# Optimization experiments

Measured on AMD Instinct MI355X. Metric: run time of the kernel, lower is better.

## Reference

```python
import jax, jax.numpy as jnp
import numpy as np

MAX_ITER = 3  # matches init max_iter
# structures exercised: sib_be, sib_bb, cop, grd, split (all distinct branches)


def _mfvi(s_const, s_arg_begin, s_arg_end,
          s_sib_be, s_sib_eb, s_sib_bb, s_sib_ee,
          s_cop_b, s_cop_e, s_grd_b, s_grd_e, s_split,
          edge_mask, chart_mask):
    B, S, _ = edge_mask.shape
    idx = jnp.arange(S)
    hs = jnp.broadcast_to(idx[:, None], (S, S))   # hs[i,j] = i (head index)
    ms = jnp.broadcast_to(idx[None, :], (S, S))   # ms[i,j] = j (modifier index)
    ls, rs = jnp.minimum(hs, ms), jnp.maximum(hs, ms)

    c0 = chart_mask[:, 0]
    pad_mask = c0[:, :, None] & c0[:, None, :]           # [B,j,k]
    chart = jnp.roll(chart_mask, 1, axis=1)              # cat((chart[:,-1:], chart[:,:-1]), 1)

    # [B,i,j,k] = edge[b,i,j] & edge[b,i,k]
    mask2o_base = edge_mask[:, :, :, None] & edge_mask[:, :, None, :]
    ne_hk = (hs[:, :, None] != idx)                      # i != k
    mask2o_wm = mask2o_base & ne_hk[None]
    mask2o = mask2o_wm & (ms[:, :, None] != idx)[None]   # additionally j != k

    lhs = ls[None, :, :] >= hs[:, :, None]               # min(j,k) >= i
    rhs = rs[None, :, :] <= hs[:, :, None]               # max(j,k) <= i
    triu_jk = idx[:, None] <= idx[None, :]               # keep k >= j (torch .triu())
    noncross = mask2o_wm & (triu_jk[None, None] & (lhs | rhs)[None])

    span_m2o = (chart[:, :, :, None]
                & (rs[:, :, None] != idx)[None]          # max(i,j) != k
                & pad_mask[:, None, :, :])
    inside = (hs[:, :, None] <= idx) & (ms[:, :, None] >= idx)  # i<=k<=... & j>=k
    outside = (~inside)[None] & span_m2o

    mzero = lambda s, m: jnp.where(m, s, 0.0)
    s_sib_be_m = mzero(s_sib_be, mask2o_wm)
    s_sib_eb_m = mzero(s_sib_eb, jnp.swapaxes(mask2o_wm, -2, -1))
    s_sib_bb_m = mzero(s_sib_bb, mask2o)
    s_sib_ee_m = mzero(s_sib_ee, mask2o)
    s_cop_b_m = mzero(s_cop_b, mask2o)
    s_cop_e_m = mzero(s_cop_e, mask2o)
    s_edge_grd_b = mzero(s_grd_b, noncross)
    s_edge_grd_e = mzero(s_grd_e, jnp.swapaxes(noncross, -2, -1))
    s_span_grd_b = mzero(jnp.transpose(s_grd_b, (0, 2, 3, 1)), outside)
    s_span_grd_e = mzero(jnp.transpose(s_grd_e, (0, 3, 2, 1)), outside)
    s_split_m = mzero(s_split, span_m2o)

    # NOTE: the torch code does `tmp_q_b = s_arg_begin; tmp_q_b += ...`, which
    # mutates the base score tensors in place, so messages ACCUMULATE into the
    # bases across iterations. We reproduce that semantics here.
    base_b, base_e, base_s = s_arg_begin, s_arg_end, s_const
    q_b, q_e, q_s = base_b, base_e, base_s
    for _ in range(MAX_ITER):
        qb = jax.nn.sigmoid(q_b)
        qe = jax.nn.sigmoid(q_e)
        qs = jax.nn.sigmoid(q_s)
        base_b = (base_b
                  + jnp.einsum('bik,bijk->bij', qe, s_sib_be_m)
                  + jnp.einsum('bik,bijk->bij', qb, s_sib_bb_m)
                  + jnp.einsum('bkj,bijk->bij', qb, s_cop_b_m)
                  + jnp.einsum('bjk,bijk->bij', qs, s_edge_grd_b))
        base_e = (base_e
                  + jnp.einsum('bik,bijk->bij', qb, s_sib_eb_m)
                  + jnp.einsum('bik,bijk->bij', qe, s_sib_ee_m)
                  + jnp.einsum('bkj,bijk->bij', qe, s_cop_e_m)
                  + jnp.einsum('bkj,bijk->bij', qs, s_edge_grd_e))
        base_s = (base_s
                  + jnp.einsum('bki,bijk->bij', qb, s_span_grd_b)
                  + jnp.einsum('bkj,bijk->bij', qe, s_span_grd_e)
                  + jnp.einsum('bik,bijk->bij', qs, s_split_m))
        q_b, q_e, q_s = base_b, base_e, base_s
    return q_b, q_e, q_s


def setup_inputs() -> dict:
    key = jax.random.key(0)
    B, S = 4, 128
    ks = jax.random.split(key, 16)
    f3 = lambda k: jax.random.normal(k, (B, S, S), jnp.float32)
    # scale 4D scores down so sums over S stay in a sane sigmoid range
    f4 = lambda k: jax.random.normal(k, (B, S, S, S), jnp.float32) * 0.05
    return {
        's_const': f3(ks[0]),
        's_arg_begin': f3(ks[1]),
        's_arg_end': f3(ks[2]),
        's_sib_be': f4(ks[3]),
        's_sib_eb': f4(ks[4]),
        's_sib_bb': f4(ks[5]),
        's_sib_ee': f4(ks[6]),
        's_cop_b': f4(ks[7]),
        's_cop_e': f4(ks[8]),
        's_grd_b': f4(ks[9]),
        's_grd_e': f4(ks[10]),
        's_split': f4(ks[11]),
        'arg_begin_mask': jax.random.bernoulli(ks[12], 0.5, (B, S, S)),
        'chart_mask': jax.random.bernoulli(ks[13], 0.5, (B, S, S)),
    }


def reference(s_const, s_arg_begin, s_arg_end,
              s_sib_be, s_sib_eb, s_sib_bb, s_sib_ee,
              s_cop_b, s_cop_e, s_grd_b, s_grd_e, s_split,
              arg_begin_mask, chart_mask):
    return _mfvi(s_const, s_arg_begin, s_arg_end,
                 s_sib_be, s_sib_eb, s_sib_bb, s_sib_ee,
                 s_cop_b, s_cop_e, s_grd_b, s_grd_e, s_split,
                 arg_begin_mask, chart_mask)
```

## Files before the change

### kernel.cpp

```cpp
#include <hip/hip_runtime.h>

#define BB 4
#define S 128
#define SS (S*S)
#define BSS (BB*SS)

__device__ __forceinline__ int off3(int b, int i, int j) { return (b * S + i) * S + j; }
__device__ __forceinline__ int off4(int b, int i, int j, int k) { return ((b * S + i) * S + j) * S + k; }

__global__ __launch_bounds__(256) void k_sigmoid(const float* __restrict__ sb,
                                                 const float* __restrict__ se,
                                                 const float* __restrict__ ss,
                                                 float* base,
                                                 float* __restrict__ ws, int init) {
    const int b = blockIdx.z, p = blockIdx.y;
    const int ti = blockIdx.x >> 2, tj = blockIdx.x & 3;
    const int col = threadIdx.x & 31, r0 = threadIdx.x >> 5;
    const float* src = (p == 0) ? sb : (p == 1) ? se : ss;

    __shared__ float tile[32][33];
#pragma unroll
    for (int rr = 0; rr < 4; ++rr) {
        const int row = r0 + 8 * rr;
        const int gi = 32 * ti + row, gj = 32 * tj + col;
        const float x = src[off3(b, gi, gj)];
        const float q = 1.0f / (1.0f + __expf(-x));
        ws[p * BSS + off3(b, gi, gj)] = q;
        if (init) base[p * BSS + off3(b, gi, gj)] = x;
        tile[row][col] = q;
    }
    __syncthreads();
#pragma unroll
    for (int rr = 0; rr < 4; ++rr) {
        const int rowo = r0 + 8 * rr;
        ws[(3 + p) * BSS + off3(b, 32 * tj + rowo, 32 * ti + col)] = tile[col][rowo];
    }
}

__global__ __launch_bounds__(256, 4) void k_terms(
    const float* __restrict__ be, const float* __restrict__ bb,
    const float* __restrict__ cb, const float* __restrict__ eb,
    const float* __restrict__ ee, const float* __restrict__ ce,
    const float* __restrict__ sp, const float* __restrict__ gb,
    const float* __restrict__ ge, const int* __restrict__ edge,
    const int* __restrict__ chart, const float* __restrict__ ws,
    float* __restrict__ base) {
    const int b = blockIdx.z, y = blockIdx.y, x = blockIdx.x;
    const int t = threadIdx.x, hw = t >> 5, lh = t & 31, l = t & 63;
    const int K = 4 * lh;

    const float* qb = ws;
    const float* qe = ws + BSS;
    const float* qs = ws + 2 * BSS;
    const float* qbT = ws + 3 * BSS;
    const float* qeT = ws + 4 * BSS;
    const float* qsT = ws + 5 * BSS;

    if (y < 7) {
        const int I = x;
        const float* A;
        int plane;
        switch (y) {
            case 0: A = be; plane = 0; break;
            case 1: A = bb; plane = 0; break;
            case 2: A = cb; plane = 0; break;
            case 3: A = eb; plane = 1; break;
            case 4: A = ee; plane = 1; break;
            case 5: A = ce; plane = 1; break;
            default: A = sp; plane = 2; break;
        }
        const int Iprev = (I + S - 1) & (S - 1);

        const bool pe0 = edge[off3(b, I, l)] != 0;
        const bool pe1 = edge[off3(b, I, 64 + l)] != 0;
        unsigned long long Mlo = __ballot(pe0), Mhi = __ballot(pe1);
        if (y == 6) {
            const bool pc0 = chart[off3(b, 0, l)] != 0;
            const bool pc1 = chart[off3(b, 0, 64 + l)] != 0;
            const bool ph0 = chart[off3(b, Iprev, l)] != 0;
            const bool ph1 = chart[off3(b, Iprev, 64 + l)] != 0;
            Mlo = __ballot(pc0) & __ballot(ph0);
            Mhi = __ballot(pc1) & __ballot(ph1);
        } else if (y == 3) {
            if (I < 64) Mlo &= ~(1ull << I);
            else Mhi &= ~(1ull << (I - 64));
        }

        const float* qrow = (y == 0 || y == 4) ? qe : (y == 1 || y == 3) ? qb : qs;
        const float4 qv = *(const float4*)&qrow[off3(b, I, K)];
        const int4 ekv = *(const int4*)&edge[off3(b, I, K)];
        const int4 c0kv = *(const int4*)&chart[off3(b, 0, K)];
        float pm[4];
        bool pmask[4];
#pragma unroll
        for (int c = 0; c < 4; ++c) {
            const bool ek = (&ekv.x)[c] != 0;
            const bool c0k = (&c0kv.x)[c] != 0;
            const bool nI = (I != K + c);
            if (y == 0 || y == 1 || y == 4) pm[c] = (ek && nI) ? (&qv.x)[c] : 0.f;
            else if (y == 3) pm[c] = ek ? (&qv.x)[c] : 0.f;
            else if (y == 6) pm[c] = c0k ? (&qv.x)[c] : 0.f;
            pmask[c] = ek && nI;
        }
        const int corrSel = (y == 1 || y == 4) ? 1 : (y == 6) ? 2 : 0;
        const float* qT3 = (y == 2) ? qbT : qeT;

        float acc[16];
        if (y == 2 || y == 5) {
#pragma unroll
            for (int jj = 0; jj < 16; ++jj) {
                const int j = 8 * jj + hw;
                const float4 v = *(const float4*)&A[off4(b, I, j, K)];
                const float4 cf = *(const float4*)&qT3[off3(b, j, K)];
                float dot = 0.f;
                float s[4];
#pragma unroll
                for (int c = 0; c < 4; ++c) {
                    s[c] = pmask[c] ? (&cf.x)[c] : 0.f;
                    dot += s[c] * (&v.x)[c];
                }
#pragma unroll
                for (int c = 0; c < 4; ++c)
                    dot -= (K + c == j) ? s[c] * (&v.x)[c] : 0.f;
                const unsigned long long M = (jj < 8) ? Mlo : Mhi;
                const bool bit = (M >> (((jj & 7) << 3) + hw)) & 1;
                acc[jj] = bit ? dot : 0.f;
            }
        } else {
#pragma unroll
            for (int jj = 0; jj < 16; ++jj) {
                const int j = 8 * jj + hw;
                const float4 v = *(const float4*)&A[off4(b, I, j, K)];
                float dot = pm[0] * v.x + pm[1] * v.y + pm[2] * v.z + pm[3] * v.w;
                const int ci = (corrSel == 0) ? 256 : (corrSel == 1) ? j : (I > j ? I : j);
#pragma unroll
                for (int c = 0; c < 4; ++c)
                    dot -= (K + c == ci) ? pm[c] * (&v.x)[c] : 0.f;
                const unsigned long long M = (jj < 8) ? Mlo : Mhi;
                const bool bit = (M >> (((jj & 7) << 3) + hw)) & 1;
                acc[jj] = bit ? dot : 0.f;
            }
        }

#pragma unroll
        for (int o = 16; o > 0; o >>= 1) {
#pragma unroll
            for (int jj = 0; jj < 16; ++jj) acc[jj] += __shfl_xor(acc[jj], o);
        }
        if (lh == 0) {
#pragma unroll
            for (int jj = 0; jj < 16; ++jj)
                atomicAdd(&base[plane * BSS + off3(b, I, 8 * jj + hw)], acc[jj]);
        }
    } else {
        const float* A = (y == 7) ? gb : ge;
        const float* qT = (y == 7) ? qbT : qeT;
        const int Jt = x & 15, Is = x >> 4;
        const int J = 8 * Jt + hw, I0 = 16 * Is;

        const float4 q_J = (y == 7) ? *(const float4*)&qs[off3(b, J, K)]
                                    : *(const float4*)&qsT[off3(b, J, K)];
        const int4 c0Kv = *(const int4*)&chart[off3(b, 0, K)];
        const bool c0J = chart[off3(b, 0, J)] != 0;
        const int Jprev = (J + S - 1) & (S - 1);
        const int4 chJKv = *(const int4*)&chart[off3(b, Jprev, K)];
        bool c0K[4], chJK[4], chKJ[4];
        int mxJ[4];
#pragma unroll
        for (int c = 0; c < 4; ++c) {
            c0K[c] = (&c0Kv.x)[c] != 0;
            chJK[c] = (&chJKv.x)[c] != 0;
            chKJ[c] = (y == 8) ? (chart[off3(b, (K + c + S - 1) & (S - 1), J)] != 0) : false;
            mxJ[c] = J > (K + c) ? J : (K + c);
        }

        const unsigned long long MeIJ = __ballot(edge[off3(b, I0 + (l & 15), J)] != 0);
        const unsigned long long Mc0I = __ballot(chart[off3(b, 0, I0 + (l & 15))] != 0);
        const int hsh = l & 32;

        float accE[16];
        float rs[4] = {0.f, 0.f, 0.f, 0.f};

#pragma unroll
        for (int s = 0; s < 16; ++s) {
            const int I = I0 + s;
            const float4 v = *(const float4*)&A[off4(b, I, J, K)];
            const int4 eIKv = *(const int4*)&edge[off3(b, I, K)];
            const bool eIJ = (MeIJ >> (hsh + s)) & 1;
            const bool c0I = (Mc0I >> (hsh + s)) & 1;
            const float qT_JI = qT[off3(b, J, I)];

            float p = 0.f;
#pragma unroll
            for (int c = 0; c < 4; ++c) {
                const int Kc = K + c;
                const bool eIK = (&eIKv.x)[c] != 0;
                const float vv = (&v.x)[c];
                bool nc, o;
                if (y == 7) {
                    nc = eIJ && eIK && (I != Kc) && (J <= Kc) && (J >= I || Kc <= I);
                    o = !((J <= I) && (Kc >= I)) && chJK[c] && (mxJ[c] != I) && c0K[c] && c0I;
                } else {
                    nc = eIK && eIJ && (I != J) && (Kc <= J) && (Kc >= I || J <= I);
                    o = !((Kc <= I) && (J >= I)) && chKJ[c] && (mxJ[c] != I) && c0J && c0I;
                }
                p += (nc ? (&q_J.x)[c] : 0.f) * vv;
                rs[c] += (o ? qT_JI : 0.f) * vv;
            }
            accE[s] = p;
        }

#pragma unroll
        for (int o = 16; o > 0; o >>= 1) {
#pragma unroll
            for (int s = 0; s < 16; ++s) accE[s] += __shfl_xor(accE[s], o);
        }
        if (lh == 0) {
#pragma unroll
            for (int s = 0; s < 16; ++s)
                atomicAdd(&base[(y == 7 ? 0 : 1) * BSS + off3(b, I0 + s, J)], accE[s]);
        }

#pragma unroll
        for (int c = 0; c < 4; ++c) {
            if (y == 7)
                atomicAdd(&base[2 * BSS + off3(b, J, K + c)], rs[c]);
            else
                atomicAdd(&base[2 * BSS + off3(b, K + c, J)], rs[c]);
        }
    }
}

extern "C" void kernel_launch(void* const* d_in, const int* in_sizes, int n_in,
                              void* d_out, int out_size, void* d_ws, size_t ws_size,
                              hipStream_t stream) {
    (void)in_sizes; (void)n_in; (void)out_size; (void)ws_size;
    const float* s_const = (const float*)d_in[0];
    const float* s_arg_begin = (const float*)d_in[1];
    const float* s_arg_end = (const float*)d_in[2];
    const float* be = (const float*)d_in[3];
    const float* eb = (const float*)d_in[4];
    const float* bb = (const float*)d_in[5];
    const float* ee = (const float*)d_in[6];
    const float* cb = (const float*)d_in[7];
    const float* ce = (const float*)d_in[8];
    const float* gb = (const float*)d_in[9];
    const float* ge = (const float*)d_in[10];
    const float* sp = (const float*)d_in[11];
    const int* edge = (const int*)d_in[12];
    const int* chart = (const int*)d_in[13];
    float* base = (float*)d_out;
    float* ws = (float*)d_ws;

    for (int it = 0; it < 3; ++it) {
        if (it == 0)
            k_sigmoid<<<dim3(16, 3, BB), dim3(256), 0, stream>>>(s_arg_begin, s_arg_end,
                                                                 s_const, base, ws, 1);
        else
            k_sigmoid<<<dim3(16, 3, BB), dim3(256), 0, stream>>>(base, base + BSS,
                                                                 base + 2 * BSS, base, ws, 0);
        k_terms<<<dim3(S, 9, BB), dim3(256), 0, stream>>>(be, bb, cb, eb, ee, ce, sp, gb, ge,
                                                          edge, chart, ws, base);
    }
}
```

Measured before the change: 500.5 us.

## Replace atomic accumulation with per-block partial planes and merge terms per row

Fuses the three per-plane score contractions sharing the same row into one block, cutting the terms grid from 9 to 5 rows of blocks and sharing the q loads. All atomicAdds into the output are replaced by plain stores into separate workspace partial planes: row sums via a shared-memory buffer, span sums as 16 slices. The sigmoid kernel then reduces those partials into the base scores. A final extra launch folds in the last iteration's partials. This removes atomic contention and makes the result deterministic, at the cost of more workspace traffic and one more launch.

```diff
diff --git a/kernel.cpp b/kernel.cpp
--- a/kernel.cpp
+++ b/kernel.cpp
@@ -5,30 +5,63 @@
 #define SS (S*S)
 #define BSS (BB*SS)
 
+#define WQ_B  0
+#define WQ_E  1
+#define WQ_S  2
+#define WQ_BT 3
+#define WQ_ET 4
+#define WQ_ST 5
+#define WP0   6
+#define WP1   7
+#define WP2   8
+#define WAE0  9
+#define WAE1  10
+#define WRS7  11
+#define WRS8  19
+
 __device__ __forceinline__ int off3(int b, int i, int j) { return (b * S + i) * S + j; }
 __device__ __forceinline__ int off4(int b, int i, int j, int k) { return ((b * S + i) * S + j) * S + k; }
 
 __global__ __launch_bounds__(256) void k_sigmoid(const float* __restrict__ sb,
                                                  const float* __restrict__ se,
                                                  const float* __restrict__ ss,
-                                                 float* base,
-                                                 float* __restrict__ ws, int init) {
+                                                 float* __restrict__ base,
+                                                 float* __restrict__ ws, int mode) {
     const int b = blockIdx.z, p = blockIdx.y;
     const int ti = blockIdx.x >> 2, tj = blockIdx.x & 3;
     const int col = threadIdx.x & 31, r0 = threadIdx.x >> 5;
-    const float* src = (p == 0) ? sb : (p == 1) ? se : ss;
-
     __shared__ float tile[32][33];
+    float* bp = base + p * BSS;
+
 #pragma unroll
     for (int rr = 0; rr < 4; ++rr) {
         const int row = r0 + 8 * rr;
         const int gi = 32 * ti + row, gj = 32 * tj + col;
-        const float x = src[off3(b, gi, gj)];
-        const float q = 1.0f / (1.0f + __expf(-x));
-        ws[p * BSS + off3(b, gi, gj)] = q;
-        if (init) base[p * BSS + off3(b, gi, gj)] = x;
-        tile[row][col] = q;
-    }
+        const int idx = off3(b, gi, gj);
+        float v;
+        if (mode == 0) {
+            const float* src = (p == 0) ? sb : (p == 1) ? se : ss;
+            v = src[idx];
+        } else {
+            v = bp[idx];
+            if (p == 0) {
+                v += ws[WP0 * BSS + idx] + ws[WAE0 * BSS + idx];
+            } else if (p == 1) {
+                v += ws[WP1 * BSS + idx] + ws[WAE1 * BSS + idx];
+            } else {
+                v += ws[WP2 * BSS + idx];
+#pragma unroll
+                for (int n = 0; n < 16; ++n) v += ws[(WRS7 + n) * BSS + idx];
+            }
+        }
+        bp[idx] = v;
+        if (mode < 2) {
+            const float q = 1.0f / (1.0f + __expf(-v));
+            ws[p * BSS + idx] = q;
+            tile[row][col] = q;
+        }
+    }
+    if (mode == 2) return;
     __syncthreads();
 #pragma unroll
     for (int rr = 0; rr < 4; ++rr) {
@@ -37,17 +70,17 @@
     }
 }
 
-__global__ __launch_bounds__(256, 4) void k_terms(
+__global__ __launch_bounds__(256) void k_terms(
     const float* __restrict__ be, const float* __restrict__ bb,
     const float* __restrict__ cb, const float* __restrict__ eb,
     const float* __restrict__ ee, const float* __restrict__ ce,
     const float* __restrict__ sp, const float* __restrict__ gb,
     const float* __restrict__ ge, const int* __restrict__ edge,
-    const int* __restrict__ chart, const float* __restrict__ ws,
-    float* __restrict__ base) {
-    const int b = blockIdx.z, y = blockIdx.y, x = blockIdx.x;
+    const int* __restrict__ chart, float* __restrict__ ws) {
+    const int b = blockIdx.z, yy = blockIdx.y, x = blockIdx.x;
     const int t = threadIdx.x, hw = t >> 5, lh = t & 31, l = t & 63;
     const int K = 4 * lh;
+    __shared__ float rowbuf[128];
 
     const float* qb = ws;
     const float* qe = ws + BSS;
@@ -56,110 +89,107 @@
     const float* qeT = ws + 4 * BSS;
     const float* qsT = ws + 5 * BSS;
 
-    if (y < 7) {
+    if (yy < 3) {
         const int I = x;
-        const float* A;
-        int plane;
-        switch (y) {
-            case 0: A = be; plane = 0; break;
-            case 1: A = bb; plane = 0; break;
-            case 2: A = cb; plane = 0; break;
-            case 3: A = eb; plane = 1; break;
-            case 4: A = ee; plane = 1; break;
-            case 5: A = ce; plane = 1; break;
-            default: A = sp; plane = 2; break;
-        }
-        const int Iprev = (I + S - 1) & (S - 1);
-
-        const bool pe0 = edge[off3(b, I, l)] != 0;
-        const bool pe1 = edge[off3(b, I, 64 + l)] != 0;
-        unsigned long long Mlo = __ballot(pe0), Mhi = __ballot(pe1);
-        if (y == 6) {
-            const bool pc0 = chart[off3(b, 0, l)] != 0;
-            const bool pc1 = chart[off3(b, 0, 64 + l)] != 0;
-            const bool ph0 = chart[off3(b, Iprev, l)] != 0;
-            const bool ph1 = chart[off3(b, Iprev, 64 + l)] != 0;
-            Mlo = __ballot(pc0) & __ballot(ph0);
-            Mhi = __ballot(pc1) & __ballot(ph1);
-        } else if (y == 3) {
-            if (I < 64) Mlo &= ~(1ull << I);
-            else Mhi &= ~(1ull << (I - 64));
-        }
-
-        const float* qrow = (y == 0 || y == 4) ? qe : (y == 1 || y == 3) ? qb : qs;
-        const float4 qv = *(const float4*)&qrow[off3(b, I, K)];
+        unsigned long long Mlo, Mhi;
+        if (yy == 2) {
+            const int Iprev = (I + S - 1) & (S - 1);
+            Mlo = __ballot(chart[off3(b, 0, l)] != 0) & __ballot(chart[off3(b, Iprev, l)] != 0);
+            Mhi = __ballot(chart[off3(b, 0, 64 + l)] != 0) & __ballot(chart[off3(b, Iprev, 64 + l)] != 0);
+        } else {
+            Mlo = __ballot(edge[off3(b, I, l)] != 0);
+            Mhi = __ballot(edge[off3(b, I, 64 + l)] != 0);
+        }
         const int4 ekv = *(const int4*)&edge[off3(b, I, K)];
-        const int4 c0kv = *(const int4*)&chart[off3(b, 0, K)];
-        float pm[4];
-        bool pmask[4];
-#pragma unroll
-        for (int c = 0; c < 4; ++c) {
-            const bool ek = (&ekv.x)[c] != 0;
-            const bool c0k = (&c0kv.x)[c] != 0;
-            const bool nI = (I != K + c);
-            if (y == 0 || y == 1 || y == 4) pm[c] = (ek && nI) ? (&qv.x)[c] : 0.f;
-            else if (y == 3) pm[c] = ek ? (&qv.x)[c] : 0.f;
-            else if (y == 6) pm[c] = c0k ? (&qv.x)[c] : 0.f;
-            pmask[c] = ek && nI;
-        }
-        const int corrSel = (y == 1 || y == 4) ? 1 : (y == 6) ? 2 : 0;
-        const float* qT3 = (y == 2) ? qbT : qeT;
-
         float acc[16];
-        if (y == 2 || y == 5) {
-#pragma unroll
-            for (int jj = 0; jj < 16; ++jj) {
-                const int j = 8 * jj + hw;
-                const float4 v = *(const float4*)&A[off4(b, I, j, K)];
+
+        if (yy == 2) {
+            const int4 c0kv = *(const int4*)&chart[off3(b, 0, K)];
+            const float4 qv = *(const float4*)&qs[off3(b, I, K)];
+            float pm[4];
+#pragma unroll
+            for (int c = 0; c < 4; ++c) pm[c] = ((&c0kv.x)[c] != 0) ? (&qv.x)[c] : 0.f;
+#pragma unroll
+            for (int jj = 0; jj < 16; ++jj) {
+                const int j = 8 * jj + hw;
+                const float4 v = *(const float4*)&sp[off4(b, I, j, K)];
+                float d = pm[0] * v.x + pm[1] * v.y + pm[2] * v.z + pm[3] * v.w;
+                const int ci = I > j ? I : j;
+#pragma unroll
+                for (int c = 0; c < 4; ++c) d -= (K + c == ci) ? pm[c] * (&v.x)[c] : 0.f;
+                acc[jj] = d;
+            }
+        } else {
+            const float4 qbv = *(const float4*)&qb[off3(b, I, K)];
+            const float4 qev = *(const float4*)&qe[off3(b, I, K)];
+            float pmA[4], pmB[4];
+            bool pmk[4];
+#pragma unroll
+            for (int c = 0; c < 4; ++c) {
+                const bool ek = (&ekv.x)[c] != 0;
+                const bool nI = (I != K + c);
+                pmk[c] = ek && nI;
+                if (yy == 0) { pmA[c] = pmk[c] ? (&qev.x)[c] : 0.f; pmB[c] = pmk[c] ? (&qbv.x)[c] : 0.f; }
+                else         { pmA[c] = ek     ? (&qbv.x)[c] : 0.f; pmB[c] = pmk[c] ? (&qev.x)[c] : 0.f; }
+            }
+            const float* A1 = (yy == 0) ? be : eb;
+            const float* A2 = (yy == 0) ? bb : ee;
+            const float* A3 = (yy == 0) ? cb : ce;
+            const float* qT3 = (yy == 0) ? qbT : qeT;
+#pragma unroll
+            for (int jj = 0; jj < 16; ++jj) {
+                const int j = 8 * jj + hw;
+                const float4 v = *(const float4*)&A1[off4(b, I, j, K)];
+                float d = pmA[0] * v.x + pmA[1] * v.y + pmA[2] * v.z + pmA[3] * v.w;
+                if (yy == 1 && j == I) d = 0.f;
+                acc[jj] = d;
+            }
+#pragma unroll
+            for (int jj = 0; jj < 16; ++jj) {
+                const int j = 8 * jj + hw;
+                const float4 v = *(const float4*)&A2[off4(b, I, j, K)];
+                float d = pmB[0] * v.x + pmB[1] * v.y + pmB[2] * v.z + pmB[3] * v.w;
+#pragma unroll
+                for (int c = 0; c < 4; ++c) d -= (K + c == j) ? pmB[c] * (&v.x)[c] : 0.f;
+                acc[jj] += d;
+            }
+#pragma unroll
+            for (int jj = 0; jj < 16; ++jj) {
+                const int j = 8 * jj + hw;
+                const float4 v = *(const float4*)&A3[off4(b, I, j, K)];
                 const float4 cf = *(const float4*)&qT3[off3(b, j, K)];
-                float dot = 0.f;
-                float s[4];
+                float d = 0.f;
 #pragma unroll
                 for (int c = 0; c < 4; ++c) {
-                    s[c] = pmask[c] ? (&cf.x)[c] : 0.f;
-                    dot += s[c] * (&v.x)[c];
+                    const float sc = pmk[c] ? (&cf.x)[c] : 0.f;
+                    d += (K + c == j) ? 0.f : sc * (&v.x)[c];
                 }
-#pragma unroll
-                for (int c = 0; c < 4; ++c)
-                    dot -= (K + c == j) ? s[c] * (&v.x)[c] : 0.f;
-                const unsigned long long M = (jj < 8) ? Mlo : Mhi;
-                const bool bit = (M >> (((jj & 7) << 3) + hw)) & 1;
-                acc[jj] = bit ? dot : 0.f;
-            }
-        } else {
-#pragma unroll
-            for (int jj = 0; jj < 16; ++jj) {
-                const int j = 8 * jj + hw;
-                const float4 v = *(const float4*)&A[off4(b, I, j, K)];
-                float dot = pm[0] * v.x + pm[1] * v.y + pm[2] * v.z + pm[3] * v.w;
-                const int ci = (corrSel == 0) ? 256 : (corrSel == 1) ? j : (I > j ? I : j);
-#pragma unroll
-                for (int c = 0; c < 4; ++c)
-                    dot -= (K + c == ci) ? pm[c] * (&v.x)[c] : 0.f;
-                const unsigned long long M = (jj < 8) ? Mlo : Mhi;
-                const bool bit = (M >> (((jj & 7) << 3) + hw)) & 1;
-                acc[jj] = bit ? dot : 0.f;
-            }
-        }
-
+                acc[jj] += d;
+            }
+        }
+
+#pragma unroll
+        for (int jj = 0; jj < 16; ++jj) {
+            const bool bit = (((jj < 8) ? Mlo : Mhi) >> (((jj & 7) << 3) + hw)) & 1;
+            acc[jj] = bit ? acc[jj] : 0.f;
+        }
 #pragma unroll
         for (int o = 16; o > 0; o >>= 1) {
 #pragma unroll
             for (int jj = 0; jj < 16; ++jj) acc[jj] += __shfl_xor(acc[jj], o);
         }
-        if (lh == 0) {
-#pragma unroll
-            for (int jj = 0; jj < 16; ++jj)
-                atomicAdd(&base[plane * BSS + off3(b, I, 8 * jj + hw)], acc[jj]);
-        }
+        if (lh < 16) rowbuf[8 * lh + hw] = acc[lh];
+        __syncthreads();
+        if (t < 32)
+            *(float4*)&ws[(WP0 + yy) * BSS + off3(b, I, 4 * t)] = *(const float4*)&rowbuf[4 * t];
     } else {
-        const float* A = (y == 7) ? gb : ge;
-        const float* qT = (y == 7) ? qbT : qeT;
+        const float* A = (yy == 3) ? gb : ge;
+        const float* qT = (yy == 3) ? qbT : qeT;
         const int Jt = x & 15, Is = x >> 4;
         const int J = 8 * Jt + hw, I0 = 16 * Is;
 
-        const float4 q_J = (y == 7) ? *(const float4*)&qs[off3(b, J, K)]
-                                    : *(const float4*)&qsT[off3(b, J, K)];
+        const float4 q_J = (yy == 3) ? *(const float4*)&qs[off3(b, J, K)]
+                                     : *(const float4*)&qsT[off3(b, J, K)];
         const int4 c0Kv = *(const int4*)&chart[off3(b, 0, K)];
         const bool c0J = chart[off3(b, 0, J)] != 0;
         const int Jprev = (J + S - 1) & (S - 1);
@@ -170,7 +200,7 @@
         for (int c = 0; c < 4; ++c) {
             c0K[c] = (&c0Kv.x)[c] != 0;
             chJK[c] = (&chJKv.x)[c] != 0;
-            chKJ[c] = (y == 8) ? (chart[off3(b, (K + c + S - 1) & (S - 1), J)] != 0) : false;
+            chKJ[c] = (yy == 4) ? (chart[off3(b, (K + c + S - 1) & (S - 1), J)] != 0) : false;
             mxJ[c] = J > (K + c) ? J : (K + c);
         }
 
@@ -190,24 +220,24 @@
             const bool c0I = (Mc0I >> (hsh + s)) & 1;
             const float qT_JI = qT[off3(b, J, I)];
 
-            float p = 0.f;
+            float p_ = 0.f;
 #pragma unroll
             for (int c = 0; c < 4; ++c) {
                 const int Kc = K + c;
                 const bool eIK = (&eIKv.x)[c] != 0;
                 const float vv = (&v.x)[c];
                 bool nc, o;
-                if (y == 7) {
+                if (yy == 3) {
                     nc = eIJ && eIK && (I != Kc) && (J <= Kc) && (J >= I || Kc <= I);
                     o = !((J <= I) && (Kc >= I)) && chJK[c] && (mxJ[c] != I) && c0K[c] && c0I;
                 } else {
                     nc = eIK && eIJ && (I != J) && (Kc <= J) && (Kc >= I || J <= I);
                     o = !((Kc <= I) && (J >= I)) && chKJ[c] && (mxJ[c] != I) && c0J && c0I;
                 }
-                p += (nc ? (&q_J.x)[c] : 0.f) * vv;
+                p_ += (nc ? (&q_J.x)[c] : 0.f) * vv;
                 rs[c] += (o ? qT_JI : 0.f) * vv;
             }
-            accE[s] = p;
+            accE[s] = p_;
         }
 
 #pragma unroll
@@ -218,15 +248,15 @@
         if (lh == 0) {
 #pragma unroll
             for (int s = 0; s < 16; ++s)
-                atomicAdd(&base[(y == 7 ? 0 : 1) * BSS + off3(b, I0 + s, J)], accE[s]);
-        }
-
-#pragma unroll
-        for (int c = 0; c < 4; ++c) {
-            if (y == 7)
-                atomicAdd(&base[2 * BSS + off3(b, J, K + c)], rs[c]);
-            else
-                atomicAdd(&base[2 * BSS + off3(b, K + c, J)], rs[c]);
+                ws[((yy == 3) ? WAE0 : WAE1) * BSS + off3(b, I0 + s, J)] = accE[s];
+        }
+        if (yy == 3) {
+            *(float4*)&ws[(WRS7 + Is) * BSS + off3(b, J, K)] =
+                make_float4(rs[0], rs[1], rs[2], rs[3]);
+        } else {
+#pragma unroll
+            for (int c = 0; c < 4; ++c)
+                ws[(WRS8 + Is) * BSS + off3(b, K + c, J)] = rs[c];
         }
     }
 }
@@ -253,13 +283,11 @@
     float* ws = (float*)d_ws;
 
     for (int it = 0; it < 3; ++it) {
-        if (it == 0)
-            k_sigmoid<<<dim3(16, 3, BB), dim3(256), 0, stream>>>(s_arg_begin, s_arg_end,
-                                                                 s_const, base, ws, 1);
-        else
-            k_sigmoid<<<dim3(16, 3, BB), dim3(256), 0, stream>>>(base, base + BSS,
-                                                                 base + 2 * BSS, base, ws, 0);
-        k_terms<<<dim3(S, 9, BB), dim3(256), 0, stream>>>(be, bb, cb, eb, ee, ce, sp, gb, ge,
-                                                          edge, chart, ws, base);
-    }
+        k_sigmoid<<<dim3(16, 3, BB), dim3(256), 0, stream>>>(s_arg_begin, s_arg_end, s_const,
+                                                             base, ws, it == 0 ? 0 : 1);
+        k_terms<<<dim3(S, 5, BB), dim3(256), 0, stream>>>(be, bb, cb, eb, ee, ce, sp, gb, ge,
+                                                          edge, chart, ws);
+    }
+    k_sigmoid<<<dim3(16, 3, BB), dim3(256), 0, stream>>>(s_arg_begin, s_arg_end, s_const,
+                                                         base, ws, 2);
 }
```

Measured after the change: 568.4 us. 13.6% more time.
